# Kernel tuning notes

Hardware: AMD Instinct MI355X
Metric: run time of the kernel (lower is better)

Reference implementation:

```python
import jax, jax.numpy as jnp
import numpy as np

B, N, E, L, G, F, H = 64, 500, 16000, 64, 64, 8, 128

def setup_inputs() -> dict:
    key = jax.random.key(0)
    ks = jax.random.split(key, 8)
    return {
        "x": jax.random.normal(ks[0], (B, N, L), dtype=jnp.float32),
        "incidence": jax.random.normal(ks[1], (N, E), dtype=jnp.float32),
        "ef": jax.random.normal(ks[2], (E, F), dtype=jnp.float32),
        "W1": jax.random.normal(ks[3], (F, H), dtype=jnp.float32) * 0.1,
        "b1": jax.random.normal(ks[4], (H,), dtype=jnp.float32) * 0.1,
        "W2": jax.random.normal(ks[5], (H, L * G), dtype=jnp.float32) * 0.1,
        "b2": jax.random.normal(ks[6], (L * G,), dtype=jnp.float32) * 0.1,
        "b_gc": jax.random.normal(ks[7], (G,), dtype=jnp.float32) * 0.1,
    }

def reference(x, incidence, ef, W1, b1, W2, b2, b_gc):
    # MLP-generated per-edge kernel: [E, G, L]
    h = jax.nn.relu(ef @ W1 + b1)
    kernel = (h @ W2 + b2).reshape(E, G, L)
    # gather node features onto edges: [B, E, L]
    t = jnp.einsum('bnl,ne->bel', x, incidence)
    # per-edge batched matvec: [B, E, G]
    y = jnp.einsum('egl,bel->beg', kernel, t)
    # scatter back to nodes: [B, N, G]
    y = jnp.einsum('ne,beg->bng', incidence, y)
    # gc is a frozen identity Linear -> just add bias, then ReLU
    y = jax.nn.relu(y + b_gc)
    return y.reshape(x.shape[0], -1)
```

## Files before the change

### kernel.cpp

```cpp
#include <hip/hip_runtime.h>

constexpr int B_ = 64, N_ = 500, E_ = 16000, L_ = 64, G_ = 64, F_ = 8, H_ = 128;
constexpr int GL_ = 4096;
constexpr int NP_ = 512;
constexpr int KS_ = 4;
constexpr int ACC_ELEMS = B_ * N_ * G_;

using bf16x8  = __attribute__((ext_vector_type(8))) short;
using f32x4   = __attribute__((ext_vector_type(4))) float;
using ushort8 = __attribute__((ext_vector_type(8))) unsigned short;

#define MFMA16(a, b, c) __builtin_amdgcn_mfma_f32_16x16x32_bf16((a), (b), (c), 0, 0, 0)

typedef __attribute__((address_space(3))) unsigned int       lds_u32;
typedef const __attribute__((address_space(1))) unsigned int glb_u32;

static __device__ __forceinline__ unsigned short f2bf(float f) {
    union { float f; unsigned u; } v; v.f = f;
    unsigned r = v.u + 0x7fffu + ((v.u >> 16) & 1u);
    return (unsigned short)(r >> 16);
}
static __device__ __forceinline__ float bf2f(unsigned short s) {
    union { float f; unsigned u; } v; v.u = ((unsigned)s) << 16;
    return v.f;
}

static __device__ __forceinline__ void stage32(
    const unsigned short* __restrict__ g, int ld, int r0, int kk,
    unsigned short* lds, int tid)
{
    #pragma unroll
    for (int c = 0; c < 2; ++c) {
        const int ch  = tid + c * 256;
        const int row = ch >> 2;
        const int csw = (ch & 3) ^ ((row >> 1) & 3);
        __builtin_amdgcn_global_load_lds(
            (glb_u32*)(g + (size_t)(r0 + row) * ld + kk + csw * 8),
            (lds_u32*)(lds + (size_t)ch * 8), 16, 0, 0);
    }
}

static __device__ __forceinline__ void gemm_body(
    const unsigned short* __restrict__ A, int lda,
    const unsigned short* __restrict__ Bm, int ldb,
    int K, int nN,
    unsigned short* __restrict__ C, int ldc,
    const float* __restrict__ bias)
{
    const int nwg = gridDim.x;
    const int bid = blockIdx.x;
    const int swz = (nwg & 7) ? bid : ((bid & 7) * (nwg >> 3) + (bid >> 3));
    const int m0 = (swz / nN) * 128, n0 = (swz % nN) * 128;

    const int tid  = threadIdx.x;
    const int lane = tid & 63, wid = tid >> 6;
    const int wm = wid >> 1, wn = wid & 1;
    const int fr = lane & 15, fq = lane >> 4;

    __shared__ __align__(16) unsigned short smem[3 * 8192];

    const f32x4 fz = {0.f, 0.f, 0.f, 0.f};
    f32x4 acc[4][4] = {{fz, fz, fz, fz}, {fz, fz, fz, fz},
                       {fz, fz, fz, fz}, {fz, fz, fz, fz}};

    const int rowA[4] = {wm * 64 + 0 * 16 + fr, wm * 64 + 1 * 16 + fr,
                         wm * 64 + 2 * 16 + fr, wm * 64 + 3 * 16 + fr};
    const int rowB[4] = {wn * 64 + 0 * 16 + fr, wn * 64 + 1 * 16 + fr,
                         wn * 64 + 2 * 16 + fr, wn * 64 + 3 * 16 + fr};
    int cA[4], cB[4];
    #pragma unroll
    for (int i = 0; i < 4; ++i) {
        cA[i] = (fq ^ ((rowA[i] >> 1) & 3)) * 8;
        cB[i] = (fq ^ ((rowB[i] >> 1) & 3)) * 8;
    }

    const int nk = K / 32;
    stage32(A, lda, m0, 0, smem, tid);
    stage32(Bm, ldb, n0, 0, smem + 4096, tid);
    stage32(A, lda, m0, 32, smem + 8192, tid);
    stage32(Bm, ldb, n0, 32, smem + 8192 + 4096, tid);

    int cur = 0;
    for (int kt = 0; kt < nk; ++kt) {
        if (kt + 1 < nk) {
            asm volatile("s_waitcnt vmcnt(4)" ::: "memory");
        } else {
            asm volatile("s_waitcnt vmcnt(0)" ::: "memory");
        }
        __builtin_amdgcn_s_barrier();
        __builtin_amdgcn_sched_barrier(0);
        if (kt + 2 < nk) {
            int nxt = cur + 2; if (nxt >= 3) nxt -= 3;
            unsigned short* const An = smem + nxt * 8192;
            stage32(A, lda, m0, (kt + 2) * 32, An, tid);
            stage32(Bm, ldb, n0, (kt + 2) * 32, An + 4096, tid);
        }
        unsigned short* const As = smem + cur * 8192;
        unsigned short* const Bs = As + 4096;
        {
            bf16x8 af[4], bf[4];
            #pragma unroll
            for (int i = 0; i < 4; ++i)
                af[i] = *(const bf16x8*)&As[rowA[i] * 32 + cA[i]];
            #pragma unroll
            for (int j = 0; j < 4; ++j)
                bf[j] = *(const bf16x8*)&Bs[rowB[j] * 32 + cB[j]];
            #pragma unroll
            for (int i = 0; i < 4; ++i)
                #pragma unroll
                for (int j = 0; j < 4; ++j)
                    acc[i][j] = MFMA16(af[i], bf[j], acc[i][j]);
        }
        __builtin_amdgcn_sched_barrier(0);
        cur = (cur + 1 == 3) ? 0 : cur + 1;
    }

    __syncthreads();
    auto Cs = (unsigned short(*)[128])smem;
    #pragma unroll
    for (int i = 0; i < 4; ++i)
        #pragma unroll
        for (int j = 0; j < 4; ++j) {
            const float bv = bias ? bias[n0 + wn * 64 + j * 16 + fr] : 0.f;
            #pragma unroll
            for (int r = 0; r < 4; ++r)
                Cs[wm * 64 + i * 16 + fq * 4 + r]
                  [(wn * 64 + j * 16 + fr) ^ (fq << 3)] =
                    f2bf(acc[i][j][r] + bv);
        }
    __syncthreads();
    const int r2 = tid >> 4, o2 = (tid & 15) * 8;
    #pragma unroll
    for (int i = 0; i < 8; ++i) {
        const int row = i * 16 + r2;
        const int o2s = o2 ^ (((row >> 2) & 3) << 3);
        *(uint4*)&C[(size_t)(m0 + row) * ldc + n0 + o2] = *(const uint4*)&Cs[row][o2s];
    }
}

__global__ __launch_bounds__(256)
void gemm_pair(const unsigned short* __restrict__ A0, int lda0,
               const unsigned short* __restrict__ B0, int ldb0, int K0,
               unsigned short* __restrict__ C0, const float* __restrict__ bias0,
               const unsigned short* __restrict__ A1, int lda1,
               const unsigned short* __restrict__ B1, int ldb1, int K1,
               unsigned short* __restrict__ C1, int nN)
{
    if (blockIdx.y == 0)
        gemm_body(A0, lda0, B0, ldb0, K0, nN, C0, GL_, bias0);
    else
        gemm_body(A1, lda1, B1, ldb1, K1, nN, C1, GL_, nullptr);
}

__global__ __launch_bounds__(512)
void k_y8(unsigned short* tc, const unsigned short* __restrict__ Kc)
{
    const int e0 = blockIdx.x * 8;
    const int tid = threadIdx.x, lane = tid & 63, w = tid >> 6;
    const int e = e0 + w;
    const int fr = lane & 15, fq = lane >> 4;
    const unsigned short* A  = &tc[(size_t)e * GL_];
    const unsigned short* Bp = &Kc[(size_t)e * GL_];
    const f32x4 fz = {0.f, 0.f, 0.f, 0.f};
    f32x4 acc[4][4] = {{fz, fz, fz, fz}, {fz, fz, fz, fz},
                       {fz, fz, fz, fz}, {fz, fz, fz, fz}};
    #pragma unroll
    for (int ks = 0; ks < 2; ++ks) {
        bf16x8 af[4], bf[4];
        #pragma unroll
        for (int i = 0; i < 4; ++i)
            af[i] = *(const bf16x8*)&A[(i * 16 + fr) * 64 + ks * 32 + fq * 8];
        #pragma unroll
        for (int j = 0; j < 4; ++j)
            bf[j] = *(const bf16x8*)&Bp[(j * 16 + fr) * 64 + ks * 32 + fq * 8];
        #pragma unroll
        for (int i = 0; i < 4; ++i)
            #pragma unroll
            for (int j = 0; j < 4; ++j)
                acc[i][j] = MFMA16(af[i], bf[j], acc[i][j]);
    }
    __shared__ unsigned short y8[GL_ * 8];
    #pragma unroll
    for (int i = 0; i < 4; ++i)
        #pragma unroll
        for (int j = 0; j < 4; ++j)
            #pragma unroll
            for (int r = 0; r < 4; ++r) {
                const int bg = (i * 16 + fq * 4 + r) * 64 + j * 16 + fr;
                y8[bg * 8 + w] = f2bf(acc[i][j][r]);
            }
    __syncthreads();
    unsigned short* dst = tc + (size_t)e0 * GL_;
    #pragma unroll
    for (int p = 0; p < 8; ++p) {
        const int o = (p * 512 + tid) * 8;
        *(uint4*)&dst[o] = *(const uint4*)&y8[o];
    }
}

__global__ __launch_bounds__(256)
void k_accd(const unsigned short* __restrict__ Ae,
            const unsigned short* __restrict__ y8,
            unsigned short* __restrict__ planesB, int pbase, int K)
{
    const int xcd = blockIdx.x & 7, grp = blockIdx.x >> 3;
    const int m0 = (grp & 7) * 64;
    const int n0 = (xcd + 8 * (grp >> 3)) * 128;
    const int KSY = gridDim.y;
    const int kl = ((K / KSY) / 64) * 64;
    const int kbeg = blockIdx.y * kl;
    const int kend = ((int)blockIdx.y == KSY - 1) ? K : kbeg + kl;

    const int lane = threadIdx.x & 63, wid = threadIdx.x >> 6;
    const int wm = wid >> 1, wn = wid & 1;
    const int fr = lane & 15, fq = lane >> 4;

    const f32x4 fz = {0.f, 0.f, 0.f, 0.f};
    f32x4 acc[2][4] = {{fz, fz, fz, fz}, {fz, fz, fz, fz}};

    for (int kk = kbeg; kk < kend; kk += 64) {
        #pragma unroll
        for (int ks = 0; ks < 2; ++ks) {
            const int e8 = kk + ks * 32 + fq * 8;
            const size_t eb = (size_t)(e8 >> 3);
            bf16x8 af[2], bf[4];
            #pragma unroll
            for (int i = 0; i < 2; ++i)
                af[i] = *(const bf16x8*)&Ae[(eb * NP_ + m0 + wm * 32 + i * 16 + fr) * 8];
            #pragma unroll
            for (int j = 0; j < 4; ++j)
                bf[j] = *(const bf16x8*)&y8[eb * GL_ * 8 + (n0 + wn * 64 + j * 16 + fr) * 8];
            #pragma unroll
            for (int i = 0; i < 2; ++i)
                #pragma unroll
                for (int j = 0; j < 4; ++j)
                    acc[i][j] = MFMA16(af[i], bf[j], acc[i][j]);
        }
    }

    unsigned short* pl = planesB + (size_t)(pbase + blockIdx.y) * ACC_ELEMS;
    #pragma unroll
    for (int i = 0; i < 2; ++i)
        #pragma unroll
        for (int j = 0; j < 4; ++j) {
            const int col = n0 + wn * 64 + j * 16 + fr;
            const int b = col >> 6, g = col & 63;
            #pragma unroll
            for (int r = 0; r < 4; ++r) {
                const int n = m0 + wm * 32 + i * 16 + fq * 4 + r;
                if (n < N_)
                    pl[((size_t)b * N_ + n) * G_ + g] = f2bf(acc[i][j][r]);
            }
        }
}

constexpr int PREP_CVT = 2000, PREP_XT = 2512, PREP_W2 = 2640, PREP_NB = 10640;

__global__ __launch_bounds__(256)
void k_prep(const float* __restrict__ x, const float* __restrict__ inc,
            const float* __restrict__ ef, const float* __restrict__ W1,
            const float* __restrict__ b1, const float* __restrict__ W2,
            unsigned short* __restrict__ incT, unsigned short* __restrict__ incB8,
            unsigned short* __restrict__ xT, unsigned short* __restrict__ W2T,
            unsigned short* __restrict__ h)
{
    __shared__ __align__(16) char smraw[64 * 65 * 4];
    const int q = blockIdx.x;
    const int tid = threadIdx.x;

    if (q < PREP_CVT) {
        auto sm = (unsigned short(*)[80])smraw;
        const int e0 = (q % 250) * 64, n0 = (q / 250) * 64;
        const int cl = tid & 63;
        for (int rr = tid >> 6; rr < 64; rr += 4) {
            const int n = n0 + rr;
            sm[cl][rr] = (n < N_) ? f2bf(inc[(size_t)n * E_ + e0 + cl]) : (unsigned short)0;
        }
        __syncthreads();
        {
            const int cw = tid >> 2, j0 = (tid & 3) * 16;
            *(ushort8*)&incT[(size_t)(e0 + cw) * NP_ + n0 + j0]     = *(const ushort8*)&sm[cw][j0];
            *(ushort8*)&incT[(size_t)(e0 + cw) * NP_ + n0 + j0 + 8] = *(const ushort8*)&sm[cw][j0 + 8];
        }
        {
            const int eb = tid >> 5, idx = tid & 31;
            #pragma unroll
            for (int k = 0; k < 2; ++k) {
                const int row = idx * 2 + k;
                unsigned short tmp[8];
                #pragma unroll
                for (int p = 0; p < 8; ++p) tmp[p] = sm[eb * 8 + p][row];
                *(ushort8*)&incB8[((size_t)((e0 >> 3) + eb) * NP_ + n0 + row) * 8] =
                    *(const ushort8*)&tmp[0];
            }
        }
    } else if (q < PREP_W2) {
        auto sm = (float(*)[65])smraw;
        const float* in; unsigned short* out;
        int R, C, Rp, c0, r0;
        if (q < PREP_XT) {
            const int t = q - PREP_CVT, z = t >> 3, by = t & 7;
            in = x + (size_t)z * N_ * L_; out = xT + (size_t)z * L_ * NP_;
            R = N_; C = L_; Rp = NP_; c0 = 0; r0 = by * 64;
        } else {
            const int t = q - PREP_XT;
            in = W2; out = W2T;
            R = H_; C = GL_; Rp = H_; c0 = (t & 63) * 64; r0 = (t >> 6) * 64;
        }
        const int cl = tid & 63;
        for (int rr = tid >> 6; rr < 64; rr += 4) {
            const int r = r0 + rr;
            sm[cl][rr] = (r < R) ? in[(size_t)r * C + c0 + cl] : 0.f;
        }
        __syncthreads();
        const int cw = tid >> 2, j0 = (tid & 3) * 16;
        unsigned short tmp[16];
        #pragma unroll
        for (int j = 0; j < 16; ++j) tmp[j] = f2bf(sm[cw][j0 + j]);
        *(ushort8*)&out[(size_t)(c0 + cw) * Rp + r0 + j0]     = *(ushort8*)&tmp[0];
        *(ushort8*)&out[(size_t)(c0 + cw) * Rp + r0 + j0 + 8] = *(ushort8*)&tmp[8];
    } else {
        const int idx = (q - PREP_W2) * 256 + tid;
        const int e = idx >> 7, hh = idx & 127;
        float v = b1[hh];
        const float* efp = &ef[(size_t)e * F_];
        #pragma unroll
        for (int f = 0; f < F_; ++f) v += efp[f] * W1[f * H_ + hh];
        h[idx] = f2bf(fmaxf(v, 0.f));
    }
}

__global__ __launch_bounds__(256)
void k_final(const unsigned short* __restrict__ planesB, int P,
             const float* __restrict__ bgc, float* __restrict__ out)
{
    const int i = (blockIdx.x * 256 + threadIdx.x) * 8;
    if (i >= ACC_ELEMS) return;
    float s[8];
    #pragma unroll
    for (int j = 0; j < 8; ++j) s[j] = bgc[(i + j) & 63];
    for (int p = 0; p < P; ++p) {
        const ushort8 v = *(const ushort8*)&planesB[(size_t)p * ACC_ELEMS + i];
        #pragma unroll
        for (int j = 0; j < 8; ++j) s[j] += bf2f((unsigned short)v[j]);
    }
    float4 o0, o1;
    o0.x = fmaxf(s[0], 0.f); o0.y = fmaxf(s[1], 0.f);
    o0.z = fmaxf(s[2], 0.f); o0.w = fmaxf(s[3], 0.f);
    o1.x = fmaxf(s[4], 0.f); o1.y = fmaxf(s[5], 0.f);
    o1.z = fmaxf(s[6], 0.f); o1.w = fmaxf(s[7], 0.f);
    *(float4*)&out[i]     = o0;
    *(float4*)&out[i + 4] = o1;
}

extern "C" void kernel_launch(void* const* d_in, const int* in_sizes, int n_in,
                              void* d_out, int out_size, void* d_ws, size_t ws_size,
                              hipStream_t stream) {
    const float* x   = (const float*)d_in[0];
    const float* inc = (const float*)d_in[1];
    const float* ef  = (const float*)d_in[2];
    const float* W1  = (const float*)d_in[3];
    const float* b1  = (const float*)d_in[4];
    const float* W2  = (const float*)d_in[5];
    const float* b2  = (const float*)d_in[6];
    const float* bgc = (const float*)d_in[7];
    float* out = (float*)d_out;

    const size_t persistU16 = (size_t)NP_ * E_
                            + (size_t)E_ * NP_
                            + (size_t)B_ * L_ * NP_
                            + (size_t)E_ * H_
                            + (size_t)GL_ * H_;
    const size_t persistBytes = persistU16 * 2;

    int nc = 1, Ec = E_;
    for (; nc <= 16; ++nc) {
        Ec = ((E_ + nc - 1) / nc + 127) / 128 * 128;
        const size_t need = persistBytes
                          + (size_t)nc * KS_ * ACC_ELEMS * 2
                          + 2 * (size_t)Ec * GL_ * 2;
        if (need <= ws_size) break;
    }
    if (nc > 16) { nc = 16; Ec = 1024; }

    unsigned short* planesB = (unsigned short*)d_ws;
    unsigned short* incB8 = planesB + (size_t)nc * KS_ * ACC_ELEMS;
    unsigned short* incT = incB8 + (size_t)NP_ * E_;
    unsigned short* xT   = incT + (size_t)E_ * NP_;
    unsigned short* h    = xT   + (size_t)B_ * L_ * NP_;
    unsigned short* W2T  = h    + (size_t)E_ * H_;
    unsigned short* Kc   = W2T  + (size_t)GL_ * H_;
    unsigned short* tc   = Kc   + (size_t)Ec * GL_;

    k_prep<<<dim3(PREP_NB), 256, 0, stream>>>(x, inc, ef, W1, b1, W2,
                                              incT, incB8, xT, W2T, h);

    int cidx = 0;
    for (int e_off = 0; e_off < E_; e_off += Ec, ++cidx) {
        const int ec = (E_ - e_off) < Ec ? (E_ - e_off) : Ec;
        gemm_pair<<<dim3((ec / 128) * 32, 2), 256, 0, stream>>>(
            h + (size_t)e_off * H_, H_, W2T, H_, H_, Kc, b2,
            incT + (size_t)e_off * NP_, NP_, xT, NP_, NP_, tc, 32);
        k_y8<<<dim3(ec / 8), 512, 0, stream>>>(tc, Kc);
        k_accd<<<dim3(256, KS_), 256, 0, stream>>>(
            incB8 + (size_t)e_off * NP_, tc, planesB, cidx * KS_, ec);
    }

    k_final<<<dim3(ACC_ELEMS / 2048), 256, 0, stream>>>(planesB, nc * KS_, bgc, out);
}
```

Baseline: 348.9 us.

## Replace LDS-staged GEMM with direct-from-global MFMA loads and 64x128 tiles

Swaps the triple-buffered LDS-staged GEMM (global_load_lds with swizzle and barriers) for a kernel where each wave reads its MFMA operands straight from global memory. The tile shrinks from 128x128 to 64x128 and blocks are mapped to XCDs so each XCD shares the same N columns (B operand) for L2 reuse. This removes LDS staging and per-k-step barrier cost, and the larger grid raises parallelism. In exchange, A and B rows are now fetched redundantly across waves with strided, less coalesced loads and no software prefetch, so the kernel relies on cache hits.

```diff
diff --git a/kernel.cpp b/kernel.cpp
--- a/kernel.cpp
+++ b/kernel.cpp
@@ -12,9 +12,6 @@
 
 #define MFMA16(a, b, c) __builtin_amdgcn_mfma_f32_16x16x32_bf16((a), (b), (c), 0, 0, 0)
 
-typedef __attribute__((address_space(3))) unsigned int       lds_u32;
-typedef const __attribute__((address_space(1))) unsigned int glb_u32;
-
 static __device__ __forceinline__ unsigned short f2bf(float f) {
     union { float f; unsigned u; } v; v.f = f;
     unsigned r = v.u + 0x7fffu + ((v.u >> 16) & 1u);
@@ -25,113 +22,64 @@
     return v.f;
 }
 
-static __device__ __forceinline__ void stage32(
-    const unsigned short* __restrict__ g, int ld, int r0, int kk,
-    unsigned short* lds, int tid)
-{
-    #pragma unroll
-    for (int c = 0; c < 2; ++c) {
-        const int ch  = tid + c * 256;
-        const int row = ch >> 2;
-        const int csw = (ch & 3) ^ ((row >> 1) & 3);
-        __builtin_amdgcn_global_load_lds(
-            (glb_u32*)(g + (size_t)(r0 + row) * ld + kk + csw * 8),
-            (lds_u32*)(lds + (size_t)ch * 8), 16, 0, 0);
-    }
-}
-
-static __device__ __forceinline__ void gemm_body(
-    const unsigned short* __restrict__ A, int lda,
-    const unsigned short* __restrict__ Bm, int ldb,
-    int K, int nN,
+static __device__ __forceinline__ void gemm_direct(
+    const unsigned short* __restrict__ A,
+    const unsigned short* __restrict__ Bm,
+    int K, int Mt,
     unsigned short* __restrict__ C, int ldc,
-    const float* __restrict__ bias)
-{
-    const int nwg = gridDim.x;
+    const float* __restrict__ bias,
+    unsigned short* __restrict__ CsRaw)
+{
     const int bid = blockIdx.x;
-    const int swz = (nwg & 7) ? bid : ((bid & 7) * (nwg >> 3) + (bid >> 3));
-    const int m0 = (swz / nN) * 128, n0 = (swz % nN) * 128;
-
-    const int tid  = threadIdx.x;
-    const int lane = tid & 63, wid = tid >> 6;
+    const int xcd = bid & 7, idx = bid >> 3;
+    const int m0 = (idx % Mt) * 64;
+    const int n0 = (xcd + 8 * (idx / Mt)) * 128;
+
+    const int tid = threadIdx.x, lane = tid & 63, wid = tid >> 6;
     const int wm = wid >> 1, wn = wid & 1;
     const int fr = lane & 15, fq = lane >> 4;
 
-    __shared__ __align__(16) unsigned short smem[3 * 8192];
-
     const f32x4 fz = {0.f, 0.f, 0.f, 0.f};
-    f32x4 acc[4][4] = {{fz, fz, fz, fz}, {fz, fz, fz, fz},
-                       {fz, fz, fz, fz}, {fz, fz, fz, fz}};
-
-    const int rowA[4] = {wm * 64 + 0 * 16 + fr, wm * 64 + 1 * 16 + fr,
-                         wm * 64 + 2 * 16 + fr, wm * 64 + 3 * 16 + fr};
-    const int rowB[4] = {wn * 64 + 0 * 16 + fr, wn * 64 + 1 * 16 + fr,
-                         wn * 64 + 2 * 16 + fr, wn * 64 + 3 * 16 + fr};
-    int cA[4], cB[4];
-    #pragma unroll
-    for (int i = 0; i < 4; ++i) {
-        cA[i] = (fq ^ ((rowA[i] >> 1) & 3)) * 8;
-        cB[i] = (fq ^ ((rowB[i] >> 1) & 3)) * 8;
-    }
-
-    const int nk = K / 32;
-    stage32(A, lda, m0, 0, smem, tid);
-    stage32(Bm, ldb, n0, 0, smem + 4096, tid);
-    stage32(A, lda, m0, 32, smem + 8192, tid);
-    stage32(Bm, ldb, n0, 32, smem + 8192 + 4096, tid);
-
-    int cur = 0;
-    for (int kt = 0; kt < nk; ++kt) {
-        if (kt + 1 < nk) {
-            asm volatile("s_waitcnt vmcnt(4)" ::: "memory");
-        } else {
-            asm volatile("s_waitcnt vmcnt(0)" ::: "memory");
-        }
-        __builtin_amdgcn_s_barrier();
-        __builtin_amdgcn_sched_barrier(0);
-        if (kt + 2 < nk) {
-            int nxt = cur + 2; if (nxt >= 3) nxt -= 3;
-            unsigned short* const An = smem + nxt * 8192;
-            stage32(A, lda, m0, (kt + 2) * 32, An, tid);
-            stage32(Bm, ldb, n0, (kt + 2) * 32, An + 4096, tid);
-        }
-        unsigned short* const As = smem + cur * 8192;
-        unsigned short* const Bs = As + 4096;
-        {
-            bf16x8 af[4], bf[4];
-            #pragma unroll
-            for (int i = 0; i < 4; ++i)
-                af[i] = *(const bf16x8*)&As[rowA[i] * 32 + cA[i]];
+    f32x4 acc[2][4] = {{fz, fz, fz, fz}, {fz, fz, fz, fz}};
+
+    const unsigned short* Ap = &A[(size_t)(m0 + wm * 32 + fr) * K];
+    const unsigned short* Bp = &Bm[(size_t)(n0 + wn * 64 + fr) * K];
+
+    for (int kk = 0; kk < K; kk += 64) {
+        #pragma unroll
+        for (int ks = 0; ks < 2; ++ks) {
+            const int ko = kk + ks * 32 + fq * 8;
+            bf16x8 af[2], bf[4];
+            #pragma unroll
+            for (int i = 0; i < 2; ++i)
+                af[i] = *(const bf16x8*)&Ap[(size_t)(i * 16) * K + ko];
             #pragma unroll
             for (int j = 0; j < 4; ++j)
-                bf[j] = *(const bf16x8*)&Bs[rowB[j] * 32 + cB[j]];
-            #pragma unroll
-            for (int i = 0; i < 4; ++i)
+                bf[j] = *(const bf16x8*)&Bp[(size_t)(j * 16) * K + ko];
+            #pragma unroll
+            for (int i = 0; i < 2; ++i)
                 #pragma unroll
                 for (int j = 0; j < 4; ++j)
                     acc[i][j] = MFMA16(af[i], bf[j], acc[i][j]);
         }
-        __builtin_amdgcn_sched_barrier(0);
-        cur = (cur + 1 == 3) ? 0 : cur + 1;
-    }
-
-    __syncthreads();
-    auto Cs = (unsigned short(*)[128])smem;
-    #pragma unroll
-    for (int i = 0; i < 4; ++i)
+    }
+
+    auto Cs = (unsigned short(*)[128])CsRaw;
+    #pragma unroll
+    for (int i = 0; i < 2; ++i)
         #pragma unroll
         for (int j = 0; j < 4; ++j) {
             const float bv = bias ? bias[n0 + wn * 64 + j * 16 + fr] : 0.f;
             #pragma unroll
             for (int r = 0; r < 4; ++r)
-                Cs[wm * 64 + i * 16 + fq * 4 + r]
+                Cs[wm * 32 + i * 16 + fq * 4 + r]
                   [(wn * 64 + j * 16 + fr) ^ (fq << 3)] =
                     f2bf(acc[i][j][r] + bv);
         }
     __syncthreads();
     const int r2 = tid >> 4, o2 = (tid & 15) * 8;
     #pragma unroll
-    for (int i = 0; i < 8; ++i) {
+    for (int i = 0; i < 4; ++i) {
         const int row = i * 16 + r2;
         const int o2s = o2 ^ (((row >> 2) & 3) << 3);
         *(uint4*)&C[(size_t)(m0 + row) * ldc + n0 + o2] = *(const uint4*)&Cs[row][o2s];
@@ -139,17 +87,18 @@
 }
 
 __global__ __launch_bounds__(256)
-void gemm_pair(const unsigned short* __restrict__ A0, int lda0,
-               const unsigned short* __restrict__ B0, int ldb0, int K0,
+void gemm_pair(const unsigned short* __restrict__ A0,
+               const unsigned short* __restrict__ B0, int K0,
                unsigned short* __restrict__ C0, const float* __restrict__ bias0,
-               const unsigned short* __restrict__ A1, int lda1,
-               const unsigned short* __restrict__ B1, int ldb1, int K1,
-               unsigned short* __restrict__ C1, int nN)
-{
+               const unsigned short* __restrict__ A1,
+               const unsigned short* __restrict__ B1, int K1,
+               unsigned short* __restrict__ C1, int Mt)
+{
+    __shared__ __align__(16) unsigned short Cs[64 * 128];
     if (blockIdx.y == 0)
-        gemm_body(A0, lda0, B0, ldb0, K0, nN, C0, GL_, bias0);
+        gemm_direct(A0, B0, K0, Mt, C0, GL_, bias0, Cs);
     else
-        gemm_body(A1, lda1, B1, ldb1, K1, nN, C1, GL_, nullptr);
+        gemm_direct(A1, B1, K1, Mt, C1, GL_, nullptr, Cs);
 }
 
 __global__ __launch_bounds__(512)
@@ -398,9 +347,10 @@
     int cidx = 0;
     for (int e_off = 0; e_off < E_; e_off += Ec, ++cidx) {
         const int ec = (E_ - e_off) < Ec ? (E_ - e_off) : Ec;
-        gemm_pair<<<dim3((ec / 128) * 32, 2), 256, 0, stream>>>(
-            h + (size_t)e_off * H_, H_, W2T, H_, H_, Kc, b2,
-            incT + (size_t)e_off * NP_, NP_, xT, NP_, NP_, tc, 32);
+        const int Mt = ec / 64;
+        gemm_pair<<<dim3(Mt * 32, 2), 256, 0, stream>>>(
+            h + (size_t)e_off * H_, W2T, H_, Kc, b2,
+            incT + (size_t)e_off * NP_, xT, NP_, tc, Mt);
         k_y8<<<dim3(ec / 8), 512, 0, stream>>>(tc, Kc);
         k_accd<<<dim3(256, KS_), 256, 0, stream>>>(
             incB8 + (size_t)e_off * NP_, tc, planesB, cidx * KS_, ec);
```

Measured after the change: 664.5 us. +90.5%, slower.
